# Kernel optimization log

Hardware: AMD Instinct MI355X
Metric: run time of the kernel (lower is better)

The kernel has to match this reference:

```python
import jax, jax.numpy as jnp
import numpy as np

N_NODES = 100000
N_EDGES = 1600000  # undirected edges (each pair listed once, no self loops)
IN_CH, HID, OUT_CH = 512, 64, 32
MU, P, K = 0.1, 1.5, 2
EPS = 1e-8


def setup_inputs() -> dict:
    key = jax.random.key(0)
    k_x, k_src, k_off, k_w1, k_w2 = jax.random.split(key, 5)
    x = jax.random.normal(k_x, (N_NODES, IN_CH), dtype=jnp.float32)
    # undirected edge list with no self loops: dst = (src + offset) % N, offset in [1, N)
    src = jax.random.randint(k_src, (N_EDGES,), 0, N_NODES)
    off = jax.random.randint(k_off, (N_EDGES,), 1, N_NODES)
    dst = (src + off) % N_NODES
    edge_index = jnp.stack([src, dst], axis=0)
    # parameters (lin1 of pGNNNet, lin1 of pGNNConv)
    W1 = jax.random.normal(k_w1, (IN_CH, HID), dtype=jnp.float32) / np.sqrt(IN_CH)
    b1 = jnp.zeros((HID,), dtype=jnp.float32)
    W2 = jax.random.normal(k_w2, (HID, OUT_CH), dtype=jnp.float32) / np.sqrt(HID)
    b2 = jnp.zeros((OUT_CH,), dtype=jnp.float32)
    return {"x": x, "edge_index": edge_index, "W1": W1, "b1": b1, "W2": W2, "b2": b2}


def reference(x, edge_index, W1, b1, W2, b2):
    src, dst = edge_index[0], edge_index[1]
    n = x.shape[0]
    # pGNNNet.lin1 + ReLU (dropout is identity in eval mode)
    h = jax.nn.relu(x @ W1 + b1)                   # [N, HID]
    # pGNNConv.lin1 applied before propagation
    f = h @ W2 + b2                                # [N, OUT]
    # degrees of the symmetric adjacency (no self loops)
    ones = jnp.ones(src.shape, dtype=f.dtype)
    deg = jax.ops.segment_sum(ones, src, num_segments=n) + \
          jax.ops.segment_sum(ones, dst, num_segments=n)
    dinv = jnp.where(deg > 0, 1.0 / deg, 0.0)      # [N]
    dis = jnp.sqrt(dinv)                           # D^{-1/2}
    out = f
    for _ in range(K):
        gs = out * dis[:, None]                    # D^{-1/2} f
        g = gs[src] - gs[dst]                      # graph gradient per edge [E, OUT]
        # edge reweighting: ||grad||^{p-2}
        w = jnp.power(jnp.sum(g * g, axis=1) + EPS, (P - 2.0) * 0.5)   # [E]
        # row sums of M (symmetric, M_ij = w_e)
        s = jax.ops.segment_sum(w, src, num_segments=n) + \
            jax.ops.segment_sum(w, dst, num_segments=n)
        alpha = 1.0 / (s * dinv + MU)              # [N]
        beta = MU * alpha
        # (D^{-1/2} M D^{-1/2} out): scatter-add messages both directions
        m = w[:, None]
        agg = jax.ops.segment_sum(m * gs[dst], src, num_segments=n) + \
              jax.ops.segment_sum(m * gs[src], dst, num_segments=n)
        out = alpha[:, None] * (dis[:, None] * agg) + beta[:, None] * f
    return jax.nn.log_softmax(out, axis=1)
```

## Files before the change

### kernel.cpp

```cpp
#include <hip/hip_runtime.h>
#include <hip/hip_bf16.h>
#include <math.h>

#define N_NODES 100000
#define N_EDGES 1600000
#define IN_CH 512
#define HID 64
#define OUT_CH 32
#define MU 0.1f
#define EPS 1e-8f

#define HE (2 * N_EDGES)
#define ABLK 625
#define EPT 20
#define NBUCK 391
#define BCAP 9216
#define PCAP 10240
#define NCAP 72

typedef short bf16x8 __attribute__((ext_vector_type(8)));
typedef unsigned short us8 __attribute__((ext_vector_type(8)));
typedef float f32x4 __attribute__((ext_vector_type(4)));

__device__ __forceinline__ short f2bf(float f) {
  __hip_bfloat16 h = __float2bfloat16(f);
  return *reinterpret_cast<short*>(&h);
}
__device__ __forceinline__ float bf2f(unsigned short u) {
  unsigned int b = ((unsigned int)u) << 16;
  return __uint_as_float(b);
}

__global__ __launch_bounds__(256) void k_scatter(
    const int* __restrict__ ends, const float* __restrict__ W1,
    const float* __restrict__ W2, short* __restrict__ w1t,
    short* __restrict__ w2t, int* __restrict__ gcur, int* __restrict__ pairs) {
  const int t = threadIdx.x;
  const int b = blockIdx.x;
  {
    const int i = b * 256 + t;
    if (i < IN_CH * HID) {
      int k = i / HID, c = i % HID;
      w1t[c * IN_CH + k] = f2bf(W1[i]);
    } else if (i < IN_CH * HID + HID * OUT_CH) {
      int j = i - IN_CH * HID;
      w2t[(j % OUT_CH) * HID + (j / OUT_CH)] = f2bf(W2[j]);
    }
  }
  __shared__ int cnt[NBUCK];
  for (int i = t; i < NBUCK; i += 256) cnt[i] = 0;
  __syncthreads();
  const int base = b * (256 * EPT);
  int us[EPT];
  #pragma unroll
  for (int j = 0; j < EPT; ++j) us[j] = ends[base + j * 256 + t];
  #pragma unroll
  for (int j = 0; j < EPT; ++j) atomicAdd(&cnt[us[j] >> 8], 1);
  __syncthreads();
  for (int i = t; i < NBUCK; i += 256) {
    const int c = cnt[i];
    cnt[i] = c > 0 ? i * BCAP + atomicAdd(&gcur[i], c) : 0;
  }
  __syncthreads();
  #pragma unroll
  for (int j = 0; j < EPT; ++j) {
    const int i = base + j * 256 + t;
    const int u = us[j];
    const int nb = ends[i < N_EDGES ? i + N_EDGES : i - N_EDGES];
    pairs[atomicAdd(&cnt[u >> 8], 1)] = ((u & 255) << 24) | nb;
  }
}

__global__ __launch_bounds__(256) void k_csr(const int* __restrict__ pairs,
                                             const int* __restrict__ gcur,
                                             int* __restrict__ degs,
                                             int* __restrict__ adj) {
  __shared__ int pl[PCAP];
  __shared__ int cnt[256];
  __shared__ int cur[256];
  const int b = blockIdx.x, t = threadIdx.x;
  const int pbase = b * BCAP;
  const int psz = gcur[b];
  const bool fits = psz <= PCAP;
  cnt[t] = 0;
  __syncthreads();
  if (fits) {
    for (int i = t; i < psz; i += 256) {
      int p = pairs[pbase + i];
      pl[i] = p;
      atomicAdd(&cnt[((unsigned)p) >> 24], 1);
    }
  } else {
    for (int i = t; i < psz; i += 256)
      atomicAdd(&cnt[((unsigned)pairs[pbase + i]) >> 24], 1);
  }
  __syncthreads();
  const int d = cnt[t];
  const int v = (b << 8) + t;
  if (v < N_NODES) degs[v] = d;
  cur[t] = v * NCAP;
  __syncthreads();
  for (int i = t; i < psz; i += 256) {
    const int p = fits ? pl[i] : pairs[pbase + i];
    adj[atomicAdd(&cur[((unsigned)p) >> 24], 1)] = p & 0xFFFFFF;
  }
  if (v < N_NODES) {
    for (int i = d; i < NCAP; ++i) adj[v * NCAP + i] = 0;
  }
}

__global__ __launch_bounds__(256) void k_mlp(
    const float* __restrict__ x, const short* __restrict__ w1t,
    const float* __restrict__ b1, const short* __restrict__ w2t,
    const float* __restrict__ b2, const int* __restrict__ degs,
    float* __restrict__ f, unsigned short* __restrict__ gs) {
  __shared__ short ht[4][16][72];
  __shared__ __align__(16) float xstage[4][2][2080];

  const int t = threadIdx.x;
  const int w = t >> 6;
  const int l = t & 63;
  const int lr = l & 15;
  const int kq = l >> 4;
  const int band = blockIdx.x * 64 + w * 16;

  const int srow = l >> 5;
  const int sgran = l & 31;

  float* bufA = xstage[w][0];
  float* bufB = xstage[w][1];
  const size_t fboff = (size_t)(lr >> 1) * 1040 + (lr & 1) * 512 + kq * 32;

  f32x4 acc1[4] = {};

  auto issue = [&](int c, float* buf) {
    #pragma unroll
    for (int i = 0; i < 8; ++i) {
      int grow = band + 2 * i + srow;
      grow = grow < N_NODES ? grow : N_NODES - 1;
      const float* gsrc = x + (size_t)grow * IN_CH + c * 128 + sgran * 4;
      __builtin_amdgcn_global_load_lds(
          (const __attribute__((address_space(1))) void*)gsrc,
          (__attribute__((address_space(3))) void*)(buf + i * 260),
          16, 0, 0);
    }
  };
  auto compute = [&](int c, const float* buf) {
    const char* fb = (const char*)buf + fboff;
    #pragma unroll
    for (int ksub = 0; ksub < 4; ++ksub) {
      const f32x4 alo = *(const f32x4*)(fb + ksub * 128);
      const f32x4 ahi = *(const f32x4*)(fb + ksub * 128 + 16);
      bf16x8 a;
      a[0] = f2bf(alo[0]); a[1] = f2bf(alo[1]); a[2] = f2bf(alo[2]); a[3] = f2bf(alo[3]);
      a[4] = f2bf(ahi[0]); a[5] = f2bf(ahi[1]); a[6] = f2bf(ahi[2]); a[7] = f2bf(ahi[3]);
      const int kg = c * 4 + ksub;
      #pragma unroll
      for (int ct = 0; ct < 4; ++ct) {
        const int cc = ct * 16 + lr;
        bf16x8 bfrag = *(const bf16x8*)&w1t[cc * IN_CH + kg * 32 + kq * 8];
        acc1[ct] = __builtin_amdgcn_mfma_f32_16x16x32_bf16(a, bfrag, acc1[ct], 0, 0, 0);
      }
    }
  };

  issue(0, bufA);
  issue(1, bufB);
  asm volatile("s_waitcnt vmcnt(0)" ::: "memory");
  compute(0, bufA);
  asm volatile("" ::: "memory");
  issue(2, bufA);
  compute(1, bufB);
  asm volatile("" ::: "memory");
  issue(3, bufB);
  asm volatile("s_waitcnt vmcnt(0)" ::: "memory");
  compute(2, bufA);
  compute(3, bufB);

  #pragma unroll
  for (int ct = 0; ct < 4; ++ct) {
    const int c = ct * 16 + lr;
    const float bb = b1[c];
    #pragma unroll
    for (int r = 0; r < 4; ++r) {
      float h = acc1[ct][r] + bb;
      ht[w][kq * 4 + r][c] = f2bf(h > 0.f ? h : 0.f);
    }
  }
  __syncthreads();

  f32x4 acc2[2] = {};
  #pragma unroll
  for (int ks = 0; ks < 2; ++ks) {
    bf16x8 a2 = *(const bf16x8*)&ht[w][lr][ks * 32 + kq * 8];
    #pragma unroll
    for (int ct = 0; ct < 2; ++ct) {
      const int c = ct * 16 + lr;
      bf16x8 bfrag = *(const bf16x8*)&w2t[c * HID + ks * 32 + kq * 8];
      acc2[ct] = __builtin_amdgcn_mfma_f32_16x16x32_bf16(a2, bfrag, acc2[ct], 0, 0, 0);
    }
  }

  #pragma unroll
  for (int r = 0; r < 4; ++r) {
    const int gr2 = band + kq * 4 + r;
    if (gr2 < N_NODES) {
      const int d = degs[gr2];
      const float di = d > 0 ? 1.0f / (float)d : 0.0f;
      const float disv = sqrtf(di);
      #pragma unroll
      for (int ct = 0; ct < 2; ++ct) {
        const int c = ct * 16 + lr;
        const float fv = acc2[ct][r] + b2[c];
        f[(size_t)gr2 * OUT_CH + c] = fv;
        gs[(size_t)gr2 * OUT_CH + c] = (unsigned short)f2bf(fv * disv);
      }
    }
  }
}

template <bool FINAL>
__global__ __launch_bounds__(256) void k_prop(
    const unsigned short* __restrict__ gs_in, const float* __restrict__ f,
    const int* __restrict__ degs, const int* __restrict__ adj,
    float* __restrict__ outf, unsigned short* __restrict__ outg) {
  const int v = blockIdx.x * 4 + (threadIdx.x >> 6);
  const int lane = threadIdx.x & 63;
  const int slot = lane >> 2;
  const int cg2 = (lane & 3) << 3;

  const int i0 = v * NCAP;
  int u[3];
  #pragma unroll
  for (int q = 0; q < 3; ++q) u[q] = adj[i0 + q * 16 + slot];
  const int dg = degs[v];
  const us8 gvu = *(const us8*)&gs_in[v * OUT_CH + cg2];
  const float4 fv0 = *(const float4*)&f[v * OUT_CH + cg2];
  const float4 fv1 = *(const float4*)&f[v * OUT_CH + cg2 + 4];

  us8 guu[3];
  #pragma unroll
  for (int q = 0; q < 3; ++q)
    guu[q] = *(const us8*)&gs_in[u[q] * OUT_CH + cg2];

  float gv[8];
  #pragma unroll
  for (int j = 0; j < 8; ++j) gv[j] = bf2f(gvu[j]);
  const float dinvv = dg > 0 ? 1.0f / (float)dg : 0.0f;
  const float disv = sqrtf(dinvv);

  float accs = 0.f;
  float acca[8] = {0.f, 0.f, 0.f, 0.f, 0.f, 0.f, 0.f, 0.f};

  #pragma unroll
  for (int q = 0; q < 3; ++q) {
    const bool vq = (q * 16 + slot) < dg;
    float gu[8];
    #pragma unroll
    for (int j = 0; j < 8; ++j) gu[j] = bf2f(guu[q][j]);
    float d = gv[0] - gu[0];
    float sq = d * d;
    #pragma unroll
    for (int j = 1; j < 8; ++j) { d = gv[j] - gu[j]; sq = fmaf(d, d, sq); }
    sq += __shfl_xor(sq, 1);
    sq += __shfl_xor(sq, 2);
    const float wq = vq ? __frsqrt_rn(sqrtf(sq + EPS)) : 0.f;
    accs += wq;
    #pragma unroll
    for (int j = 0; j < 8; ++j) acca[j] = fmaf(wq, gu[j], acca[j]);
  }
  for (int base = 48; base < dg; base += 16) {
    const int idx = base + slot;
    const bool vq = idx < dg;
    const int ut = vq ? adj[i0 + idx] : v;
    const us8 gut = *(const us8*)&gs_in[ut * OUT_CH + cg2];
    float gu[8];
    #pragma unroll
    for (int j = 0; j < 8; ++j) gu[j] = bf2f(gut[j]);
    float d = gv[0] - gu[0];
    float sq = d * d;
    #pragma unroll
    for (int j = 1; j < 8; ++j) { d = gv[j] - gu[j]; sq = fmaf(d, d, sq); }
    sq += __shfl_xor(sq, 1);
    sq += __shfl_xor(sq, 2);
    const float wq = vq ? __frsqrt_rn(sqrtf(sq + EPS)) : 0.f;
    accs += wq;
    #pragma unroll
    for (int j = 0; j < 8; ++j) acca[j] = fmaf(wq, gu[j], acca[j]);
  }

  #pragma unroll
  for (int s = 4; s <= 32; s <<= 1) {
    accs += __shfl_xor(accs, s);
    #pragma unroll
    for (int j = 0; j < 8; ++j) acca[j] += __shfl_xor(acca[j], s);
  }

  const float alpha = 1.0f / (accs * dinvv + MU);
  const float ad = alpha * disv;
  const float ba = MU * alpha;
  float r[8];
  r[0] = fmaf(ad, acca[0], ba * fv0.x);
  r[1] = fmaf(ad, acca[1], ba * fv0.y);
  r[2] = fmaf(ad, acca[2], ba * fv0.z);
  r[3] = fmaf(ad, acca[3], ba * fv0.w);
  r[4] = fmaf(ad, acca[4], ba * fv1.x);
  r[5] = fmaf(ad, acca[5], ba * fv1.y);
  r[6] = fmaf(ad, acca[6], ba * fv1.z);
  r[7] = fmaf(ad, acca[7], ba * fv1.w);

  if (FINAL) {
    float m = r[0];
    #pragma unroll
    for (int j = 1; j < 8; ++j) m = fmaxf(m, r[j]);
    m = fmaxf(m, __shfl_xor(m, 1));
    m = fmaxf(m, __shfl_xor(m, 2));
    float se = 0.f;
    #pragma unroll
    for (int j = 0; j < 8; ++j) se += __expf(r[j] - m);
    se += __shfl_xor(se, 1);
    se += __shfl_xor(se, 2);
    const float lse = m + __logf(se);
    if (slot == 0) {
      float4 o0 = make_float4(r[0] - lse, r[1] - lse, r[2] - lse, r[3] - lse);
      float4 o1 = make_float4(r[4] - lse, r[5] - lse, r[6] - lse, r[7] - lse);
      *(float4*)&outf[v * OUT_CH + cg2] = o0;
      *(float4*)&outf[v * OUT_CH + cg2 + 4] = o1;
    }
  } else {
    if (slot == 0) {
      us8 o;
      #pragma unroll
      for (int j = 0; j < 8; ++j) o[j] = (unsigned short)f2bf(r[j] * disv);
      *(us8*)&outg[v * OUT_CH + cg2] = o;
    }
  }
}

extern "C" void kernel_launch(void* const* d_in, const int* in_sizes, int n_in,
                              void* d_out, int out_size, void* d_ws, size_t ws_size,
                              hipStream_t stream) {
  const float* x = (const float*)d_in[0];
  const int* ei = (const int*)d_in[1];
  const float* W1 = (const float*)d_in[2];
  const float* b1 = (const float*)d_in[3];
  const float* W2 = (const float*)d_in[4];
  const float* b2 = (const float*)d_in[5];
  float* out = (float*)d_out;

  float* f = (float*)d_ws;
  unsigned short* gsa = (unsigned short*)(f + (size_t)N_NODES * 32);
  unsigned short* gsb = gsa + (size_t)N_NODES * 32;
  int* degs = (int*)(gsb + (size_t)N_NODES * 32);
  int* adj = degs + N_NODES;
  short* w1t = (short*)(adj + (size_t)N_NODES * NCAP);
  short* w2t = w1t + IN_CH * HID;
  int* gcur = (int*)(w2t + HID * OUT_CH);
  int* pairs = (int*)f;

  hipMemsetAsync(gcur, 0, NBUCK * sizeof(int), stream);
  k_scatter<<<ABLK, 256, 0, stream>>>(ei, W1, W2, w1t, w2t, gcur, pairs);
  k_csr<<<NBUCK, 256, 0, stream>>>(pairs, gcur, degs, adj);
  k_mlp<<<(N_NODES + 63) / 64, 256, 0, stream>>>(x, w1t, b1, w2t, b2, degs, f, gsa);
  k_prop<false><<<N_NODES / 4, 256, 0, stream>>>(gsa, f, degs, adj, nullptr, gsb);
  k_prop<true><<<N_NODES / 4, 256, 0, stream>>>(gsb, f, degs, adj, out, nullptr);
}
```

Measured before the change: 260.7 us.

## Single-buffer MLP x staging and drop adjacency padding zero-fill

The MLP kernel's double-buffered LDS staging of x is replaced by a single buffer per wave, loaded and consumed chunk by chunk with a full wait between. This halves LDS use, which may allow more resident blocks, but gives up overlap of global loads with MFMA compute. The adjacency build no longer zero-fills unused slots. Instead the propagation kernel clamps out-of-range neighbor indices to 0 before gathering, which saves stores but reads uninitialized slots that are masked later.

```diff
diff --git a/kernel.cpp b/kernel.cpp
--- a/kernel.cpp
+++ b/kernel.cpp
@@ -95,17 +95,13 @@
       atomicAdd(&cnt[((unsigned)pairs[pbase + i]) >> 24], 1);
   }
   __syncthreads();
-  const int d = cnt[t];
   const int v = (b << 8) + t;
-  if (v < N_NODES) degs[v] = d;
+  if (v < N_NODES) degs[v] = cnt[t];
   cur[t] = v * NCAP;
   __syncthreads();
   for (int i = t; i < psz; i += 256) {
     const int p = fits ? pl[i] : pairs[pbase + i];
     adj[atomicAdd(&cur[((unsigned)p) >> 24], 1)] = p & 0xFFFFFF;
-  }
-  if (v < N_NODES) {
-    for (int i = d; i < NCAP; ++i) adj[v * NCAP + i] = 0;
   }
 }
 
@@ -115,7 +111,7 @@
     const float* __restrict__ b2, const int* __restrict__ degs,
     float* __restrict__ f, unsigned short* __restrict__ gs) {
   __shared__ short ht[4][16][72];
-  __shared__ __align__(16) float xstage[4][2][2080];
+  __shared__ __align__(16) float xstage[4][2080];
 
   const int t = threadIdx.x;
   const int w = t >> 6;
@@ -124,16 +120,15 @@
   const int kq = l >> 4;
   const int band = blockIdx.x * 64 + w * 16;
 
+  float* xb = xstage[w];
   const int srow = l >> 5;
   const int sgran = l & 31;
 
-  float* bufA = xstage[w][0];
-  float* bufB = xstage[w][1];
-  const size_t fboff = (size_t)(lr >> 1) * 1040 + (lr & 1) * 512 + kq * 32;
-
   f32x4 acc1[4] = {};
-
-  auto issue = [&](int c, float* buf) {
+  const char* fb = (const char*)xb + (lr >> 1) * 1040 + (lr & 1) * 512 + kq * 32;
+
+  for (int c = 0; c < 4; ++c) {
+    asm volatile("" ::: "memory");
     #pragma unroll
     for (int i = 0; i < 8; ++i) {
       int grow = band + 2 * i + srow;
@@ -141,12 +136,10 @@
       const float* gsrc = x + (size_t)grow * IN_CH + c * 128 + sgran * 4;
       __builtin_amdgcn_global_load_lds(
           (const __attribute__((address_space(1))) void*)gsrc,
-          (__attribute__((address_space(3))) void*)(buf + i * 260),
+          (__attribute__((address_space(3))) void*)(xb + i * 260),
           16, 0, 0);
     }
-  };
-  auto compute = [&](int c, const float* buf) {
-    const char* fb = (const char*)buf + fboff;
+    asm volatile("s_waitcnt vmcnt(0)" ::: "memory");
     #pragma unroll
     for (int ksub = 0; ksub < 4; ++ksub) {
       const f32x4 alo = *(const f32x4*)(fb + ksub * 128);
@@ -162,20 +155,7 @@
         acc1[ct] = __builtin_amdgcn_mfma_f32_16x16x32_bf16(a, bfrag, acc1[ct], 0, 0, 0);
       }
     }
-  };
-
-  issue(0, bufA);
-  issue(1, bufB);
-  asm volatile("s_waitcnt vmcnt(0)" ::: "memory");
-  compute(0, bufA);
-  asm volatile("" ::: "memory");
-  issue(2, bufA);
-  compute(1, bufB);
-  asm volatile("" ::: "memory");
-  issue(3, bufB);
-  asm volatile("s_waitcnt vmcnt(0)" ::: "memory");
-  compute(2, bufA);
-  compute(3, bufB);
+  }
 
   #pragma unroll
   for (int ct = 0; ct < 4; ++ct) {
@@ -238,6 +218,10 @@
   const float4 fv0 = *(const float4*)&f[v * OUT_CH + cg2];
   const float4 fv1 = *(const float4*)&f[v * OUT_CH + cg2 + 4];
 
+  #pragma unroll
+  for (int q = 0; q < 3; ++q)
+    u[q] = (unsigned)u[q] < N_NODES ? u[q] : 0;
+
   us8 guu[3];
   #pragma unroll
   for (int q = 0; q < 3; ++q)
```

Result: faster. 242.8 us (-6.9%).
